# Performance work log

Measured on AMD Instinct MI355X. Metric: run time of the kernel, lower is better.

The kernel has to match this reference:

```python
import jax, jax.numpy as jnp
import numpy as np

S = 128           # seq_len
B = 256           # input_bits (bits per token, also neurons per head)
H = 16            # num_heads
NB = 12           # n_bits_per_neuron -> LUT size 2^12
PB = 7            # relative-position bits = ceil(log2(max_seq_len))
HEAD_IN = 2 * B + PB   # concat(query, key, rel_pos_bits) = 519
THRESH = H // 2


def setup_inputs() -> dict:
    key = jax.random.key(0)
    k1, k2, k3 = jax.random.split(key, 3)
    tokens = jax.random.randint(k1, (S, B), 0, 2, dtype=jnp.int32)           # binary token bits
    memory = jax.random.normal(k2, (H, B, 2 ** NB), dtype=jnp.float32)       # RAM LUT contents per head/neuron
    connections = jax.random.randint(k3, (H, B, NB), 0, HEAD_IN, dtype=jnp.int32)  # per-neuron input-bit wiring
    return {"tokens": tokens, "memory": memory, "connections": connections}


def reference(tokens, memory, connections):
    idx = jnp.arange(S)
    rel = idx[:, None] - idx[None, :]                         # [S,S] i - j
    mask = (rel >= 0).astype(jnp.int32)                        # causal mask (j <= i)
    relc = jnp.clip(rel, 0, S - 1)
    # relative-distance binary encoding, LSB first: [S,S,PB]
    pos_bits = ((relc[..., None] >> jnp.arange(PB)) & 1).astype(jnp.int32)
    q = jnp.broadcast_to(tokens[:, None, :], (S, S, B))
    k = jnp.broadcast_to(tokens[None, :, :], (S, S, B))
    head_in = jnp.concatenate([q, k, pos_bits], axis=-1)       # [S,S,HEAD_IN]
    # RAM address per (query i, key j, head h, neuron n): pack NB wired bits, LSB first
    addr = jnp.zeros((S, S, H, B), dtype=jnp.int32)
    for b in range(NB):  # tiny fixed loop over bit planes, fully vectorized over S,S,H,B
        addr = addr + (head_in[..., connections[:, :, b]] << b)
    # LUT gather: memory[h, n, addr] -> [S,S,H,B]
    h_idx = jnp.arange(H)[:, None]
    n_idx = jnp.arange(B)[None, :]
    vals = memory[h_idx, n_idx, addr]
    bits = (vals > 0.0).astype(jnp.int32)                      # RAM neuron output bit
    # XOR accumulation over attended keys == masked sum mod 2: [S,H,B]
    head_res = jnp.sum(bits * mask[:, :, None, None], axis=1) % 2
    # majority vote across heads per bit
    ones_count = jnp.sum(head_res, axis=1)                     # [S,B]
    return (ones_count > THRESH).astype(jnp.int32)
```

## Files before the change

kernel.cpp:

```cpp
#include <hip/hip_runtime.h>


#define S 128
#define B 256
#define H 16
#define NB 12

__device__ __forceinline__ unsigned sig(unsigned x) {
    return x ^ ((x >> 3) & 0x70u) ^ ((x >> 6) & 0x70u);
}

#define TW(c) ((((c) & 3) << 1) + ((c) >> 7))
#define TP(c) (((c) >> 2) & 31)

__global__ __launch_bounds__(256) void pack_kernel(
    const int* __restrict__ tokens,
    unsigned* __restrict__ tokP)
{
    const int wid  = threadIdx.x >> 6;
    const int lane = threadIdx.x & 63;
    const int4* tp = (const int4*)tokens;
    #pragma unroll
    for (int r = 0; r < 4; ++r) {
        int i = blockIdx.x * 16 + wid * 4 + r;
        int4 x = tp[i * 64 + lane];
        unsigned long long B0 = __ballot((x.x & 1) != 0);
        unsigned long long B1 = __ballot((x.y & 1) != 0);
        unsigned long long B2 = __ballot((x.z & 1) != 0);
        unsigned long long B3 = __ballot((x.w & 1) != 0);
        int c = lane >> 1;
        unsigned long long s01 = (c & 1) ? B1 : B0;
        unsigned long long s23 = (c & 1) ? B3 : B2;
        unsigned long long s   = (c & 2) ? s23 : s01;
        unsigned word = (lane & 1) ? (unsigned)(s >> 32) : (unsigned)s;
        if (lane < 8) tokP[lane * 128 + i] = word;
    }
}

__global__ __launch_bounds__(256, 4) void softram_kernel(
    const unsigned* __restrict__ tokP,
    const float* __restrict__ memory,
    const int* __restrict__ connections,
    unsigned char* __restrict__ pc)
{
    const int bid  = blockIdx.x;
    const int g    = bid >> 8;
    const int n    = bid & 255;
    const int tid  = threadIdx.x;
    const int wid  = tid >> 6;
    const int hg   = g * 4 + wid;
    const int lane = tid & 63;

    __shared__ __align__(16) unsigned char  bytetab[4 * 4096];
    __shared__ __align__(16) unsigned int   tokT[8 * S];
    __shared__ __align__(16) unsigned short akT[4][S];
    __shared__ __align__(16) unsigned short apt[4][S];
    __shared__ int            conns[4][NB];
    __shared__ unsigned int   parts[4][4];

    const float4* mrow = (const float4*)(memory + ((size_t)(hg * 256 + n) << 12));
    float4 va[16];
    #pragma unroll
    for (int t = 0; t < 16; ++t) va[t] = mrow[lane + 64 * t];

    ((int4*)tokT)[tid] = ((const int4*)tokP)[tid];
    if (tid < 4 * NB) {
        int hh = tid / NB, b = tid - hh * NB;
        conns[hh][b] = connections[(size_t)(g * 4 + hh) * (B * NB) + n * NB + b];
    }
    __syncthreads();

    unsigned qmask = 0, kmask = 0, pmask = 0;
    #pragma unroll
    for (int b = 0; b < NB; ++b) {
        int c = conns[wid][b];
        qmask |= (unsigned)(c < 256) << b;
        kmask |= (unsigned)(c >= 256 && c < 512) << b;
        pmask |= (unsigned)(c >= 512) << b;
    }
    const int qb = __popc(qmask);
    const int kb = __popc(kmask);

    unsigned char* __restrict__ bt = &bytetab[wid << 12];
    unsigned long long rlo = 0, rhi = 0;

    if (pmask == 0) {
        unsigned qclsA = 0, qclsB = 0;
        #pragma unroll
        for (int e = 0; e < 2; ++e) {
            int ii = lane + 64 * e;
            unsigned qc = 0, kc = 0;
            int qn = 0, kn = 0;
            #pragma unroll
            for (int b = 0; b < NB; ++b) {
                int c = conns[wid][b];
                if (c < 256) {
                    qc |= ((tokT[TW(c) * S + ii] >> TP(c)) & 1u) << qn;
                    ++qn;
                } else {
                    int c2 = c - 256;
                    kc |= ((tokT[TW(c2) * S + ii] >> TP(c2)) & 1u) << kn;
                    ++kn;
                }
            }
            akT[wid][ii] = (unsigned short)kc;
            if (e == 0) qclsA = qc; else qclsB = qc;
        }

        #pragma unroll
        for (int t = 0; t < 16; ++t) {
            float4 v = va[t];
            unsigned p = 4u * (unsigned)(lane + 64 * t);
            unsigned w = (unsigned)(v.x > 0.f)
                       | ((unsigned)(v.y > 0.f) << 8)
                       | ((unsigned)(v.z > 0.f) << 16)
                       | ((unsigned)(v.w > 0.f) << 24);
            *(unsigned*)&bt[sig(p)] = w;
        }

        const bool formA = (qb <= 6);
        const int SBITS  = formA ? qb : kb;
        unsigned apl = 0, aul = 0;
        {
            int scnt = 0, lcnt = 0;
            #pragma unroll
            for (int b = 0; b < NB; ++b) {
                int c = conns[wid][b];
                bool isS = formA ? (c < 256) : (c >= 256);
                if (isS) {
                    apl |= (((unsigned)lane >> scnt) & 1u) << b;
                    ++scnt;
                } else {
                    int p = SBITS + lcnt;
                    if (p < 6) apl |= (((unsigned)lane >> p) & 1u) << b;
                    else       aul |= (((unsigned)lane >> (p - 6)) & 1u) << b;
                    ++lcnt;
                }
            }
        }
        const unsigned spl  = sig(apl);
        const unsigned saul = sig(aul);
        unsigned Wlo = 0, Whi = 0;
        #pragma unroll 8
        for (int it = 0; it < 64; ++it) {
            unsigned sau  = (unsigned)__builtin_amdgcn_readlane((int)saul, it);
            unsigned bitv = bt[sau ^ spl] & 1u;
            unsigned long long Bm = __ballot(bitv != 0u);
#if __has_builtin(__builtin_amdgcn_writelane)
            Wlo = (unsigned)__builtin_amdgcn_writelane((int)(unsigned)Bm, it, (int)Wlo);
            Whi = (unsigned)__builtin_amdgcn_writelane((int)(unsigned)(Bm >> 32), it, (int)Whi);
#else
            Wlo = (lane == it) ? (unsigned)Bm : Wlo;
            Whi = (lane == it) ? (unsigned)(Bm >> 32) : Whi;
#endif
        }
        const unsigned long long Wfull = ((unsigned long long)Whi << 32) | Wlo;

        if (formA) {
            unsigned kclsA = akT[wid][lane];
            unsigned g0 = kclsA << qb;
            unsigned long long V = __shfl(Wfull, (int)(g0 >> 6)) >> (g0 & 63u);
            #pragma unroll
            for (int d = 1; d < 64; d <<= 1) {
                unsigned long long u = __shfl_up(V, (unsigned)d);
                V ^= (lane >= d) ? u : 0ull;
            }
            rlo = __ballot(((V >> qclsA) & 1ull) != 0ull);
            const unsigned long long Abase = __shfl(V, 63);

            unsigned kclsB = akT[wid][64 + lane];
            unsigned g1 = kclsB << qb;
            unsigned long long V1 = __shfl(Wfull, (int)(g1 >> 6)) >> (g1 & 63u);
            #pragma unroll
            for (int d = 1; d < 64; d <<= 1) {
                unsigned long long u = __shfl_up(V1, (unsigned)d);
                V1 ^= (lane >= d) ? u : 0ull;
            }
            V1 ^= Abase;
            rhi = __ballot(((V1 >> qclsB) & 1ull) != 0ull);
        } else {
            unsigned kclsA = akT[wid][lane];
            unsigned C = 1u << kclsA;
            #pragma unroll
            for (int d = 1; d < 64; d <<= 1) {
                unsigned u = __shfl_up(C, (unsigned)d);
                C ^= (lane >= d) ? u : 0u;
            }
            unsigned g0a = qclsA << kb;
            unsigned W0 = (unsigned)(__shfl(Wfull, (int)(g0a >> 6)) >> (g0a & 63u));
            rlo = __ballot((__popc(W0 & C) & 1) != 0);
            const unsigned Cbase = __shfl(C, 63);

            unsigned kclsB = akT[wid][64 + lane];
            unsigned C1 = 1u << kclsB;
            #pragma unroll
            for (int d = 1; d < 64; d <<= 1) {
                unsigned u = __shfl_up(C1, (unsigned)d);
                C1 ^= (lane >= d) ? u : 0u;
            }
            C1 ^= Cbase;
            unsigned g0b = qclsB << kb;
            unsigned W1 = (unsigned)(__shfl(Wfull, (int)(g0b >> 6)) >> (g0b & 63u));
            rhi = __ballot((__popc(W1 & C1) & 1) != 0);
        }
    } else {
        unsigned aqv0 = 0, aqv1 = 0;
        #pragma unroll
        for (int e = 0; e < 2; ++e) {
            int ii = lane + 64 * e;
            unsigned aq = 0, ak = 0, ap = 0;
            #pragma unroll
            for (int b = 0; b < NB; ++b) {
                int c = conns[wid][b];
                if (c < 256) {
                    aq |= ((tokT[TW(c) * S + ii] >> TP(c)) & 1u) << b;
                } else if (c < 512) {
                    int c2 = c - 256;
                    ak |= ((tokT[TW(c2) * S + ii] >> TP(c2)) & 1u) << b;
                } else {
                    ap |= (((unsigned)ii >> (c - 512)) & 1u) << b;
                }
            }
            akT[wid][ii] = (unsigned short)sig(ak);
            apt[wid][ii] = (unsigned short)sig(ap);
            if (e == 0) aqv0 = sig(aq); else aqv1 = sig(aq);
        }

        #pragma unroll
        for (int t = 0; t < 16; ++t) {
            float4 v = va[t];
            unsigned p = 4u * (unsigned)(lane + 64 * t);
            unsigned w = (unsigned)(v.x > 0.f)
                       | ((unsigned)(v.y > 0.f) << 8)
                       | ((unsigned)(v.z > 0.f) << 16)
                       | ((unsigned)(v.w > 0.f) << 24);
            *(unsigned*)&bt[sig(p)] = w;
        }

        unsigned acc0 = 0, acc1 = 0;
        for (int s8 = 0; s8 < 8; ++s8) {
            uint4 uk = *(const uint4*)&akT[wid][s8 * 8];
            #pragma unroll
            for (int t = 0; t < 8; ++t) {
                int j = s8 * 8 + t;
                unsigned w = ((const unsigned*)&uk)[t >> 1];
                unsigned akv = (w >> ((t & 1) * 16)) & 0xffffu;
                int d0 = lane - j;
                unsigned v0 = bt[aqv0 ^ akv ^ (unsigned)apt[wid][d0 & 127]] & 1u;
                acc0 ^= (d0 >= 0) ? v0 : 0u;
                int d1 = lane + 64 - j;
                unsigned v1 = bt[aqv1 ^ akv ^ (unsigned)apt[wid][d1]] & 1u;
                acc1 ^= v1;
            }
        }
        for (int s8 = 8; s8 < 16; ++s8) {
            uint4 uk = *(const uint4*)&akT[wid][s8 * 8];
            #pragma unroll
            for (int t = 0; t < 8; ++t) {
                int j = s8 * 8 + t;
                unsigned w = ((const unsigned*)&uk)[t >> 1];
                unsigned akv = (w >> ((t & 1) * 16)) & 0xffffu;
                int d1 = lane + 64 - j;
                unsigned v1 = bt[aqv1 ^ akv ^ (unsigned)apt[wid][d1 & 127]] & 1u;
                acc1 ^= (d1 >= 0) ? v1 : 0u;
            }
        }
        rlo = __ballot(acc0 != 0u);
        rhi = __ballot(acc1 != 0u);
    }

    if (lane == 0) {
        parts[wid][0] = (unsigned)rlo;
        parts[wid][1] = (unsigned)(rlo >> 32);
        parts[wid][2] = (unsigned)rhi;
        parts[wid][3] = (unsigned)(rhi >> 32);
    }
    __syncthreads();

    if (tid < S) {
        int i = tid, tot = 0;
        #pragma unroll
        for (int hh = 0; hh < 4; ++hh)
            tot += (parts[hh][i >> 5] >> (i & 31)) & 1;
        pc[((size_t)g * 256 + n) * 128 + i] = (unsigned char)tot;
    }
}

__global__ __launch_bounds__(128) void vote_kernel(
    const unsigned char* __restrict__ pc,
    int* __restrict__ out)
{
    const int n = blockIdx.x;
    const int i = threadIdx.x;
    int tot = pc[(size_t)(0 * 256 + n) * 128 + i]
            + pc[(size_t)(1 * 256 + n) * 128 + i]
            + pc[(size_t)(2 * 256 + n) * 128 + i]
            + pc[(size_t)(3 * 256 + n) * 128 + i];
    out[i * B + n] = (tot > (H / 2)) ? 1 : 0;
}

extern "C" void kernel_launch(void* const* d_in, const int* in_sizes, int n_in,
                              void* d_out, int out_size, void* d_ws, size_t ws_size,
                              hipStream_t stream) {
    const int*   tokens      = (const int*)d_in[0];
    const float* memory      = (const float*)d_in[1];
    const int*   connections = (const int*)d_in[2];
    int*         out         = (int*)d_out;
    unsigned char* pc        = (unsigned char*)d_ws;
    unsigned*      tokP      = (unsigned*)((char*)d_ws + 4 * 256 * 128);
    (void)in_sizes; (void)n_in; (void)out_size; (void)ws_size;

    pack_kernel<<<8, 256, 0, stream>>>(tokens, tokP);
    softram_kernel<<<4 * B, 256, 0, stream>>>(tokP, memory, connections, pc);
    vote_kernel<<<B, 128, 0, stream>>>(pc, out);
}
```

Baseline: 110.0 us.

## Split softram blocks into producer/consumer warps with LDS flag handoff

Each block now handles two (head, neuron) rows. Two producer waves stream the LUT memory row with a short rolling prefetch and build the byte table. Two consumer waves compute key/query address classes in parallel, then spin on an LDS flag before doing the lookups. This aims to overlap the global memory load with address setup, cut per-thread register pressure so more blocks fit per CU, and move the per-head reduction into the vote kernel as 64-bit bitmasks. The risks are the spin-wait correctness relying on LDS ordering, and half the waves sitting idle after they finish producing.

```diff
diff --git a/kernel.cpp b/kernel.cpp
--- a/kernel.cpp
+++ b/kernel.cpp
@@ -37,55 +37,71 @@
     }
 }
 
-__global__ __launch_bounds__(256, 4) void softram_kernel(
+__global__ __launch_bounds__(256, 8) void softram_kernel(
     const unsigned* __restrict__ tokP,
     const float* __restrict__ memory,
     const int* __restrict__ connections,
-    unsigned char* __restrict__ pc)
+    unsigned long long* __restrict__ pres)
 {
-    const int bid  = blockIdx.x;
-    const int g    = bid >> 8;
-    const int n    = bid & 255;
     const int tid  = threadIdx.x;
     const int wid  = tid >> 6;
-    const int hg   = g * 4 + wid;
     const int lane = tid & 63;
-
-    __shared__ __align__(16) unsigned char  bytetab[4 * 4096];
+    const bool producer = (wid < 2);
+    const int s = producer ? wid : (wid - 2);
+    const int r = blockIdx.x * 2 + s;
+
+    __shared__ __align__(16) unsigned char  bytetab[2][4096];
     __shared__ __align__(16) unsigned int   tokT[8 * S];
-    __shared__ __align__(16) unsigned short akT[4][S];
-    __shared__ __align__(16) unsigned short apt[4][S];
-    __shared__ int            conns[4][NB];
-    __shared__ unsigned int   parts[4][4];
-
-    const float4* mrow = (const float4*)(memory + ((size_t)(hg * 256 + n) << 12));
-    float4 va[16];
+    __shared__ __align__(16) unsigned short akT[2][S];
+    __shared__ __align__(16) unsigned short apt[2][S];
+    __shared__ int flag[2];
+
+    int c_l = 0;
+    if (!producer && lane < NB) c_l = connections[(size_t)r * NB + lane];
+    ((int4*)tokT)[tid] = ((const int4*)tokP)[tid];
+    if (tid < 2) flag[tid] = 0;
+    __syncthreads();
+
+    unsigned char* __restrict__ bt = bytetab[s];
+
+    if (producer) {
+        const float4* mp = (const float4*)(memory + ((size_t)r << 12));
+        float4 va[4];
+        #pragma unroll
+        for (int t = 0; t < 4; ++t) va[t] = mp[lane + 64 * t];
+        #pragma unroll
+        for (int t = 0; t < 16; ++t) {
+            float4 v = va[t & 3];
+            if (t + 4 < 16) va[t & 3] = mp[lane + 64 * (t + 4)];
+            unsigned w = (unsigned)(v.x > 0.f)
+                       | ((unsigned)(v.y > 0.f) << 8)
+                       | ((unsigned)(v.z > 0.f) << 16)
+                       | ((unsigned)(v.w > 0.f) << 24);
+            *(unsigned*)&bt[sig(4u * (unsigned)(lane + 64 * t))] = w;
+        }
+        asm volatile("s_waitcnt lgkmcnt(0)" ::: "memory");
+        if (lane == 0) *(volatile int*)&flag[s] = 1;
+        return;
+    }
+
+    int cb[NB];
     #pragma unroll
-    for (int t = 0; t < 16; ++t) va[t] = mrow[lane + 64 * t];
-
-    ((int4*)tokT)[tid] = ((const int4*)tokP)[tid];
-    if (tid < 4 * NB) {
-        int hh = tid / NB, b = tid - hh * NB;
-        conns[hh][b] = connections[(size_t)(g * 4 + hh) * (B * NB) + n * NB + b];
-    }
-    __syncthreads();
+    for (int b = 0; b < NB; ++b)
+        cb[b] = __builtin_amdgcn_readfirstlane(__shfl(c_l, b));
 
     unsigned qmask = 0, kmask = 0, pmask = 0;
     #pragma unroll
     for (int b = 0; b < NB; ++b) {
-        int c = conns[wid][b];
-        qmask |= (unsigned)(c < 256) << b;
-        kmask |= (unsigned)(c >= 256 && c < 512) << b;
-        pmask |= (unsigned)(c >= 512) << b;
+        qmask |= (unsigned)(cb[b] < 256) << b;
+        kmask |= (unsigned)(cb[b] >= 256 && cb[b] < 512) << b;
+        pmask |= (unsigned)(cb[b] >= 512) << b;
     }
     const int qb = __popc(qmask);
     const int kb = __popc(kmask);
-
-    unsigned char* __restrict__ bt = &bytetab[wid << 12];
-    unsigned long long rlo = 0, rhi = 0;
-
-    if (pmask == 0) {
-        unsigned qclsA = 0, qclsB = 0;
+    const bool fast = (pmask == 0);
+
+    unsigned qclsA = 0, qclsB = 0;
+    if (fast) {
         #pragma unroll
         for (int e = 0; e < 2; ++e) {
             int ii = lane + 64 * e;
@@ -93,7 +109,7 @@
             int qn = 0, kn = 0;
             #pragma unroll
             for (int b = 0; b < NB; ++b) {
-                int c = conns[wid][b];
+                int c = cb[b];
                 if (c < 256) {
                     qc |= ((tokT[TW(c) * S + ii] >> TP(c)) & 1u) << qn;
                     ++qn;
@@ -103,21 +119,39 @@
                     ++kn;
                 }
             }
-            akT[wid][ii] = (unsigned short)kc;
+            akT[s][ii] = (unsigned short)kc;
             if (e == 0) qclsA = qc; else qclsB = qc;
         }
-
+    } else {
         #pragma unroll
-        for (int t = 0; t < 16; ++t) {
-            float4 v = va[t];
-            unsigned p = 4u * (unsigned)(lane + 64 * t);
-            unsigned w = (unsigned)(v.x > 0.f)
-                       | ((unsigned)(v.y > 0.f) << 8)
-                       | ((unsigned)(v.z > 0.f) << 16)
-                       | ((unsigned)(v.w > 0.f) << 24);
-            *(unsigned*)&bt[sig(p)] = w;
-        }
-
+        for (int e = 0; e < 2; ++e) {
+            int ii = lane + 64 * e;
+            unsigned aq = 0, ak = 0, ap = 0;
+            #pragma unroll
+            for (int b = 0; b < NB; ++b) {
+                int c = cb[b];
+                if (c < 256) {
+                    aq |= ((tokT[TW(c) * S + ii] >> TP(c)) & 1u) << b;
+                } else if (c < 512) {
+                    int c2 = c - 256;
+                    ak |= ((tokT[TW(c2) * S + ii] >> TP(c2)) & 1u) << b;
+                } else {
+                    ap |= (((unsigned)ii >> (c - 512)) & 1u) << b;
+                }
+            }
+            akT[s][ii] = (unsigned short)sig(ak);
+            apt[s][ii] = (unsigned short)sig(ap);
+            if (e == 0) qclsA = sig(aq); else qclsB = sig(aq);
+        }
+    }
+
+    while (*(volatile int*)&flag[s] == 0) __builtin_amdgcn_s_sleep(2);
+    asm volatile("" ::: "memory");
+    __builtin_amdgcn_sched_barrier(0);
+
+    unsigned long long rlo = 0, rhi = 0;
+
+    if (fast) {
         const bool formA = (qb <= 6);
         const int SBITS  = formA ? qb : kb;
         unsigned apl = 0, aul = 0;
@@ -125,7 +159,7 @@
             int scnt = 0, lcnt = 0;
             #pragma unroll
             for (int b = 0; b < NB; ++b) {
-                int c = conns[wid][b];
+                int c = cb[b];
                 bool isS = formA ? (c < 256) : (c >= 256);
                 if (isS) {
                     apl |= (((unsigned)lane >> scnt) & 1u) << b;
@@ -157,7 +191,7 @@
         const unsigned long long Wfull = ((unsigned long long)Whi << 32) | Wlo;
 
         if (formA) {
-            unsigned kclsA = akT[wid][lane];
+            unsigned kclsA = akT[s][lane];
             unsigned g0 = kclsA << qb;
             unsigned long long V = __shfl(Wfull, (int)(g0 >> 6)) >> (g0 & 63u);
             #pragma unroll
@@ -168,7 +202,7 @@
             rlo = __ballot(((V >> qclsA) & 1ull) != 0ull);
             const unsigned long long Abase = __shfl(V, 63);
 
-            unsigned kclsB = akT[wid][64 + lane];
+            unsigned kclsB = akT[s][64 + lane];
             unsigned g1 = kclsB << qb;
             unsigned long long V1 = __shfl(Wfull, (int)(g1 >> 6)) >> (g1 & 63u);
             #pragma unroll
@@ -179,7 +213,7 @@
             V1 ^= Abase;
             rhi = __ballot(((V1 >> qclsB) & 1ull) != 0ull);
         } else {
-            unsigned kclsA = akT[wid][lane];
+            unsigned kclsA = akT[s][lane];
             unsigned C = 1u << kclsA;
             #pragma unroll
             for (int d = 1; d < 64; d <<= 1) {
@@ -191,7 +225,7 @@
             rlo = __ballot((__popc(W0 & C) & 1) != 0);
             const unsigned Cbase = __shfl(C, 63);
 
-            unsigned kclsB = akT[wid][64 + lane];
+            unsigned kclsB = akT[s][64 + lane];
             unsigned C1 = 1u << kclsB;
             #pragma unroll
             for (int d = 1; d < 64; d <<= 1) {
@@ -204,64 +238,32 @@
             rhi = __ballot((__popc(W1 & C1) & 1) != 0);
         }
     } else {
-        unsigned aqv0 = 0, aqv1 = 0;
-        #pragma unroll
-        for (int e = 0; e < 2; ++e) {
-            int ii = lane + 64 * e;
-            unsigned aq = 0, ak = 0, ap = 0;
-            #pragma unroll
-            for (int b = 0; b < NB; ++b) {
-                int c = conns[wid][b];
-                if (c < 256) {
-                    aq |= ((tokT[TW(c) * S + ii] >> TP(c)) & 1u) << b;
-                } else if (c < 512) {
-                    int c2 = c - 256;
-                    ak |= ((tokT[TW(c2) * S + ii] >> TP(c2)) & 1u) << b;
-                } else {
-                    ap |= (((unsigned)ii >> (c - 512)) & 1u) << b;
-                }
-            }
-            akT[wid][ii] = (unsigned short)sig(ak);
-            apt[wid][ii] = (unsigned short)sig(ap);
-            if (e == 0) aqv0 = sig(aq); else aqv1 = sig(aq);
-        }
-
-        #pragma unroll
-        for (int t = 0; t < 16; ++t) {
-            float4 v = va[t];
-            unsigned p = 4u * (unsigned)(lane + 64 * t);
-            unsigned w = (unsigned)(v.x > 0.f)
-                       | ((unsigned)(v.y > 0.f) << 8)
-                       | ((unsigned)(v.z > 0.f) << 16)
-                       | ((unsigned)(v.w > 0.f) << 24);
-            *(unsigned*)&bt[sig(p)] = w;
-        }
-
+        const unsigned aqv0 = qclsA, aqv1 = qclsB;
         unsigned acc0 = 0, acc1 = 0;
         for (int s8 = 0; s8 < 8; ++s8) {
-            uint4 uk = *(const uint4*)&akT[wid][s8 * 8];
+            uint4 uk = *(const uint4*)&akT[s][s8 * 8];
             #pragma unroll
             for (int t = 0; t < 8; ++t) {
                 int j = s8 * 8 + t;
                 unsigned w = ((const unsigned*)&uk)[t >> 1];
                 unsigned akv = (w >> ((t & 1) * 16)) & 0xffffu;
                 int d0 = lane - j;
-                unsigned v0 = bt[aqv0 ^ akv ^ (unsigned)apt[wid][d0 & 127]] & 1u;
+                unsigned v0 = bt[aqv0 ^ akv ^ (unsigned)apt[s][d0 & 127]] & 1u;
                 acc0 ^= (d0 >= 0) ? v0 : 0u;
                 int d1 = lane + 64 - j;
-                unsigned v1 = bt[aqv1 ^ akv ^ (unsigned)apt[wid][d1]] & 1u;
+                unsigned v1 = bt[aqv1 ^ akv ^ (unsigned)apt[s][d1]] & 1u;
                 acc1 ^= v1;
             }
         }
         for (int s8 = 8; s8 < 16; ++s8) {
-            uint4 uk = *(const uint4*)&akT[wid][s8 * 8];
+            uint4 uk = *(const uint4*)&akT[s][s8 * 8];
             #pragma unroll
             for (int t = 0; t < 8; ++t) {
                 int j = s8 * 8 + t;
                 unsigned w = ((const unsigned*)&uk)[t >> 1];
                 unsigned akv = (w >> ((t & 1) * 16)) & 0xffffu;
                 int d1 = lane + 64 - j;
-                unsigned v1 = bt[aqv1 ^ akv ^ (unsigned)apt[wid][d1 & 127]] & 1u;
+                unsigned v1 = bt[aqv1 ^ akv ^ (unsigned)apt[s][d1 & 127]] & 1u;
                 acc1 ^= (d1 >= 0) ? v1 : 0u;
             }
         }
@@ -270,32 +272,22 @@
     }
 
     if (lane == 0) {
-        parts[wid][0] = (unsigned)rlo;
-        parts[wid][1] = (unsigned)(rlo >> 32);
-        parts[wid][2] = (unsigned)rhi;
-        parts[wid][3] = (unsigned)(rhi >> 32);
-    }
-    __syncthreads();
-
-    if (tid < S) {
-        int i = tid, tot = 0;
-        #pragma unroll
-        for (int hh = 0; hh < 4; ++hh)
-            tot += (parts[hh][i >> 5] >> (i & 31)) & 1;
-        pc[((size_t)g * 256 + n) * 128 + i] = (unsigned char)tot;
+        pres[(size_t)r * 2 + 0] = rlo;
+        pres[(size_t)r * 2 + 1] = rhi;
     }
 }
 
 __global__ __launch_bounds__(128) void vote_kernel(
-    const unsigned char* __restrict__ pc,
+    const unsigned long long* __restrict__ pres,
     int* __restrict__ out)
 {
     const int n = blockIdx.x;
     const int i = threadIdx.x;
-    int tot = pc[(size_t)(0 * 256 + n) * 128 + i]
-            + pc[(size_t)(1 * 256 + n) * 128 + i]
-            + pc[(size_t)(2 * 256 + n) * 128 + i]
-            + pc[(size_t)(3 * 256 + n) * 128 + i];
+    const int w = i >> 6, b = i & 63;
+    int tot = 0;
+    #pragma unroll
+    for (int h = 0; h < H; ++h)
+        tot += (int)((pres[(size_t)(h * 256 + n) * 2 + w] >> b) & 1ull);
     out[i * B + n] = (tot > (H / 2)) ? 1 : 0;
 }
 
@@ -306,11 +298,11 @@
     const float* memory      = (const float*)d_in[1];
     const int*   connections = (const int*)d_in[2];
     int*         out         = (int*)d_out;
-    unsigned char* pc        = (unsigned char*)d_ws;
-    unsigned*      tokP      = (unsigned*)((char*)d_ws + 4 * 256 * 128);
+    unsigned long long* pres = (unsigned long long*)d_ws;
+    unsigned*           tokP = (unsigned*)((char*)d_ws + (64u << 10));
     (void)in_sizes; (void)n_in; (void)out_size; (void)ws_size;
 
     pack_kernel<<<8, 256, 0, stream>>>(tokens, tokP);
-    softram_kernel<<<4 * B, 256, 0, stream>>>(tokP, memory, connections, pc);
-    vote_kernel<<<B, 128, 0, stream>>>(pc, out);
-}
+    softram_kernel<<<2048, 256, 0, stream>>>(tokP, memory, connections, pres);
+    vote_kernel<<<B, 128, 0, stream>>>(pres, out);
+}
```

Result: faster. 107.1 us (-2.6%).
